# Performance work log

Hardware: AMD Instinct MI355X
Metric: run time of the kernel (lower is better)

The kernel has to match this reference:

```python
import jax, jax.numpy as jnp
import numpy as np

B, C, H, W = 8, 256, 64, 64
D = C // 8  # query/key channels


def setup_inputs() -> dict:
    key = jax.random.key(0)
    ks = jax.random.split(key, 7)
    s = 0.05
    x = jax.random.normal(ks[0], (B, C, H, W), dtype=jnp.float32)
    Wq = jax.random.normal(ks[1], (D, C), dtype=jnp.float32) * s
    bq = jax.random.normal(ks[2], (D,), dtype=jnp.float32) * s
    Wk = jax.random.normal(ks[3], (D, C), dtype=jnp.float32) * s
    bk = jax.random.normal(ks[4], (D,), dtype=jnp.float32) * s
    Wv = jax.random.normal(ks[5], (C, C), dtype=jnp.float32) * s
    bv = jax.random.normal(ks[6], (C,), dtype=jnp.float32) * s
    return {"x": x, "Wq": Wq, "bq": bq, "Wk": Wk, "bk": bk, "Wv": Wv, "bv": bv}


def reference(x, Wq, bq, Wk, bk, Wv, bv):
    b, c, h, w = x.shape
    n = h * w
    xf = x.reshape(b, c, n)  # (B, C, HW)
    # 1x1 convs == per-pixel linear projections
    q = jnp.einsum('dc,bcn->bdn', Wq, xf) + bq[None, :, None]  # (B, D, HW)
    k = jnp.einsum('dc,bcn->bdn', Wk, xf) + bk[None, :, None]  # (B, D, HW)
    v = jnp.einsum('ec,bcn->ben', Wv, xf) + bv[None, :, None]  # (B, C, HW)
    # attention[b, n, m] = sum_d q[b,d,n] * k[b,d,m]  (no 1/sqrt(d) scaling)
    attn = jax.nn.softmax(jnp.einsum('bdn,bdm->bnm', q, k), axis=-1)
    # out[b,c,n] = sum_m v[b,c,m] * attn[b,n,m]  (v @ attn^T)
    out = jnp.einsum('bcm,bnm->bcn', v, attn)
    return out.reshape(b, c, h, w) + x
```

## Files before the change

### kernel.cpp

```cpp
#include <hip/hip_runtime.h>
#include <stdint.h>

#define BN 4096
#define NCH 256
#define DQ 32

typedef _Float16 half8  __attribute__((ext_vector_type(8)));
typedef _Float16 half4  __attribute__((ext_vector_type(4)));
typedef _Float16 half2  __attribute__((ext_vector_type(2)));
typedef float   floatx4  __attribute__((ext_vector_type(4)));
typedef float   floatx16 __attribute__((ext_vector_type(16)));

typedef __attribute__((address_space(1))) const void g1_void;
typedef __attribute__((address_space(3))) void l3_void;

#define LOG2E 1.44269504088896f
#define EXP2F(x) __builtin_amdgcn_exp2f(x)
#define LOG2F(x) __builtin_amdgcn_logf(x)

__global__ __launch_bounds__(256) void convert_w(
    const float* __restrict__ Wq, const float* __restrict__ Wk,
    const float* __restrict__ Wv, _Float16* __restrict__ W16)
{
    int e4 = (blockIdx.x * 256 + threadIdx.x) * 4;
    float4 v;
    if (e4 < 8192)        v = *(const float4*)&Wq[e4];
    else if (e4 < 16384) {
        v = *(const float4*)&Wk[e4 - 8192];
        v.x *= LOG2E; v.y *= LOG2E; v.z *= LOG2E; v.w *= LOG2E;
    }
    else                  v = *(const float4*)&Wv[e4 - 16384];
    half4 h = { (_Float16)v.x, (_Float16)v.y, (_Float16)v.z, (_Float16)v.w };
    *(half4*)&W16[e4] = h;
}

__global__ __launch_bounds__(512) void proj_kernel(
    const float* __restrict__ x, const _Float16* __restrict__ W16,
    const float* __restrict__ bq, const float* __restrict__ bk,
    const float* __restrict__ bv,
    _Float16* __restrict__ qT, _Float16* __restrict__ kT,
    _Float16* __restrict__ vb)
{
    const int t  = threadIdx.x;
    const int n0 = blockIdx.x * 128;
    const int b  = blockIdx.y;

    __shared__ __align__(16) _Float16 xTl[128 * 256];

#pragma unroll
    for (int p = 0; p < 2; ++p) {
        const int kb = p * 128 + (t >> 5) * 8;
        const int n4 = (t & 31) * 4;
        float4 xr[8];
#pragma unroll
        for (int i = 0; i < 8; ++i)
            xr[i] = *(const float4*)&x[((size_t)b * NCH + kb + i) * BN + n0 + n4];
        const float* xf = (const float*)xr;
#pragma unroll
        for (int j = 0; j < 4; ++j) {
            const int n = n4 + j;
            half8 hv;
#pragma unroll
            for (int i = 0; i < 8; ++i) hv[i] = (_Float16)xf[i * 4 + j];
            const int phys = (kb >> 3) ^ ((n >> 2) & 31);
            *(half8*)&xTl[n * 256 + phys * 8] = hv;
        }
    }
    __syncthreads();

    const int lane  = t & 63;
    const int w     = t >> 6;
    const int col32 = lane & 31;
    const int h     = lane >> 5;
    const int nc    = w & 3;
    const int job   = w >> 2;

    const _Float16* Wq16 = W16;
    const _Float16* Wk16 = W16 + 8192;
    const _Float16* Wv16 = W16 + 16384;

#define XFRAG(ks) (*(const half8*)&xTl[(nc * 32 + col32) * 256 + \
        (((ks) * 2 + h) ^ (((nc * 32 + col32) >> 2) & 31)) * 8])

    if (job == 0) {
        const float bqv = bq[col32];
        const float bkv = bk[col32] * LOG2E;
        floatx16 aq, ak2;
#pragma unroll
        for (int r = 0; r < 16; ++r) { aq[r] = 0.0f; ak2[r] = 0.0f; }
#pragma unroll
        for (int ks = 0; ks < 16; ++ks) {
            half8 xa = XFRAG(ks);
            half8 wqf = *(const half8*)&Wq16[col32 * 256 + ks * 16 + h * 8];
            half8 wkf = *(const half8*)&Wk16[col32 * 256 + ks * 16 + h * 8];
            aq  = __builtin_amdgcn_mfma_f32_32x32x16_f16(xa, wqf, aq, 0, 0, 0);
            ak2 = __builtin_amdgcn_mfma_f32_32x32x16_f16(xa, wkf, ak2, 0, 0, 0);
        }
#pragma unroll
        for (int r = 0; r < 16; ++r) {
            const int n = n0 + nc * 32 + (r & 3) + 8 * (r >> 2) + 4 * h;
            qT[((size_t)b * BN + n) * DQ + col32] = (_Float16)(aq[r] + bqv);
            kT[((size_t)b * BN + n) * DQ + col32] = (_Float16)(ak2[r] + bkv);
        }
    }

    const int rg_lo = (job == 0) ? 0 : 3;
    const int rg_hi = (job == 0) ? 3 : 8;
    for (int rg = rg_lo; rg < rg_hi; ++rg) {
        floatx16 av;
#pragma unroll
        for (int r = 0; r < 16; ++r) av[r] = 0.0f;
#pragma unroll
        for (int ks = 0; ks < 16; ++ks) {
            half8 xb  = XFRAG(ks);
            half8 wvf = *(const half8*)&Wv16[(rg * 32 + col32) * 256 + ks * 16 + h * 8];
            av = __builtin_amdgcn_mfma_f32_32x32x16_f16(wvf, xb, av, 0, 0, 0);
        }
#pragma unroll
        for (int r = 0; r < 16; ++r) {
            const int c = rg * 32 + (r & 3) + 8 * (r >> 2) + 4 * h;
            vb[((size_t)b * NCH + c) * BN + n0 + nc * 32 + col32] =
                (_Float16)(av[r] + bv[c]);
        }
    }
#undef XFRAG
}

__global__ __launch_bounds__(256, 3) void flash_kernel(
    const _Float16* __restrict__ qT, const _Float16* __restrict__ kT,
    const _Float16* __restrict__ vb,
    _Float16* __restrict__ Op, float* __restrict__ Ml, int KPS)
{
    const int t    = threadIdx.x;
    const int lane = t & 63;
    const int w    = t >> 6;
    const int n0   = blockIdx.x * 64;
    const int kh   = blockIdx.y;
    const int b    = blockIdx.z;
    const int kbase = kh * KPS;
    const int iters = (min(KPS, BN - kbase)) >> 6;

    __shared__ __align__(16) _Float16 vs[NCH * 64];
    __shared__ __align__(16) _Float16 Ps[2][64 * 64];
    __shared__ float alph_s[2][64];
    __shared__ float l_s[64];

    const int col   = lane & 15;
    const int q4    = lane >> 4;
    const int col32 = lane & 31;
    const int h     = lane >> 5;

    const _Float16* kp = kT + (size_t)b * BN * DQ;
    const _Float16* vp = vb + (size_t)b * NCH * BN;

    half8 bqf = *(const half8*)&qT[((size_t)b * BN + n0 + w * 16 + col) * DQ + q4 * 8];

    floatx16 acc[2][2];
#pragma unroll
    for (int ct = 0; ct < 2; ++ct)
#pragma unroll
        for (int nt = 0; nt < 2; ++nt)
#pragma unroll
            for (int r = 0; r < 16; ++r) acc[ct][nt][r] = 0.0f;

    float m_i = -1e30f, l_i = 0.0f;

    const int sc_loc = lane >> 3;
    const int s_log  = (lane & 7) ^ (sc_loc & 7);
    half8 ak[4];
#pragma unroll
    for (int mt = 0; mt < 4; ++mt)
        ak[mt] = *(const half8*)&kp[(size_t)(kbase + mt * 16 + col) * DQ + q4 * 8];
#pragma unroll
    for (int j = 0; j < 8; ++j) {
        const int c = w * 64 + j * 8 + sc_loc;
        __builtin_amdgcn_global_load_lds(
            (g1_void*)&vp[(size_t)c * BN + kbase + s_log * 8],
            (l3_void*)&vs[(w * 64 + j * 8) * 64], 16, 0, 0);
    }

    for (int it = 0; it < iters; ++it) {
        const int mc  = kbase + it * 64;
        const int cur = it & 1;

        floatx4 sf[4];
        __builtin_amdgcn_s_setprio(1);
#pragma unroll
        for (int mt = 0; mt < 4; ++mt) {
            floatx4 z = { 0.0f, 0.0f, 0.0f, 0.0f };
            sf[mt] = __builtin_amdgcn_mfma_f32_16x16x32_f16(ak[mt], bqf, z, 0, 0, 0);
        }
        __builtin_amdgcn_s_setprio(0);

        {
            const int mcn = (it + 1 < iters) ? mc + 64 : mc;
#pragma unroll
            for (int mt = 0; mt < 4; ++mt)
                ak[mt] = *(const half8*)&kp[(size_t)(mcn + mt * 16 + col) * DQ + q4 * 8];
        }

        float cmax = -1e30f;
#pragma unroll
        for (int mt = 0; mt < 4; ++mt)
#pragma unroll
            for (int r = 0; r < 4; ++r) cmax = fmaxf(cmax, sf[mt][r]);
        cmax = fmaxf(cmax, __shfl_xor(cmax, 16));
        cmax = fmaxf(cmax, __shfl_xor(cmax, 32));
        const float mn = (cmax > m_i + 8.0f) ? cmax : m_i;
        float al = EXP2F(m_i - mn);
        float csum = 0.0f;
        half4 pk[4];
#pragma unroll
        for (int mt = 0; mt < 4; ++mt) {
            float p0 = EXP2F(sf[mt][0] - mn);
            float p1 = EXP2F(sf[mt][1] - mn);
            float p2 = EXP2F(sf[mt][2] - mn);
            float p3 = EXP2F(sf[mt][3] - mn);
            csum += p0 + p1 + p2 + p3;
            half2 q01 = __builtin_bit_cast(half2, __builtin_amdgcn_cvt_pkrtz(p0, p1));
            half2 q23 = __builtin_bit_cast(half2, __builtin_amdgcn_cvt_pkrtz(p2, p3));
            half4 pkv;
            pkv[0] = q01[0]; pkv[1] = q01[1];
            pkv[2] = q23[0]; pkv[3] = q23[1];
            pk[mt] = pkv;
        }
        csum += __shfl_xor(csum, 16);
        csum += __shfl_xor(csum, 32);
        l_i = l_i * al + csum;
        m_i = mn;

        {
            const int n = w * 16 + col;
#pragma unroll
            for (int mt = 0; mt < 4; ++mt) {
                const int p_log = 2 * mt + (q4 >> 1);
                const int p_phys = p_log ^ (n & 7);
                *(half4*)((char*)&Ps[cur][n * 64] + p_phys * 16 + (q4 & 1) * 8) = pk[mt];
            }
            if (q4 == 0) alph_s[cur][n] = al;
        }

        asm volatile("s_waitcnt lgkmcnt(0)" ::: "memory");
        __builtin_amdgcn_s_barrier();

        float a0 = alph_s[cur][col32];
        float a1 = alph_s[cur][32 + col32];
        if (!__all((a0 == 1.0f) && (a1 == 1.0f))) {
#pragma unroll
            for (int ct = 0; ct < 2; ++ct)
#pragma unroll
                for (int r = 0; r < 16; ++r) {
                    acc[ct][0][r] *= a0;
                    acc[ct][1][r] *= a1;
                }
        }

        asm volatile("s_waitcnt vmcnt(4)" ::: "memory");

        __builtin_amdgcn_s_setprio(1);
#pragma unroll
        for (int ks = 0; ks < 4; ++ks) {
            const int p_log = 2 * ks + h;
            half8 bp0 = *(const half8*)((char*)&Ps[cur][col32 * 64] + (p_log ^ (col32 & 7)) * 16);
            half8 bp1 = *(const half8*)((char*)&Ps[cur][(32 + col32) * 64] + (p_log ^ (col32 & 7)) * 16);
#pragma unroll
            for (int ct = 0; ct < 2; ++ct) {
                const int c = w * 64 + ct * 32 + col32;
                half8 av = *(const half8*)((char*)&vs[c * 64] + ((p_log ^ (c & 7)) * 16));
                acc[ct][0] = __builtin_amdgcn_mfma_f32_32x32x16_f16(av, bp0, acc[ct][0], 0, 0, 0);
                acc[ct][1] = __builtin_amdgcn_mfma_f32_32x32x16_f16(av, bp1, acc[ct][1], 0, 0, 0);
            }
        }
        __builtin_amdgcn_s_setprio(0);

        if (it + 1 < iters) {
            asm volatile("s_waitcnt lgkmcnt(0)" ::: "memory");
            const int mcn = mc + 64;
#pragma unroll
            for (int j = 0; j < 8; ++j) {
                const int c = w * 64 + j * 8 + sc_loc;
                __builtin_amdgcn_global_load_lds(
                    (g1_void*)&vp[(size_t)c * BN + mcn + s_log * 8],
                    (l3_void*)&vs[(w * 64 + j * 8) * 64], 16, 0, 0);
            }
        }
    }

    if (q4 == 0) {
        const int n = w * 16 + col;
        l_s[n] = l_i;
        Ml[(size_t)(kh * 8 + b) * BN + n0 + n] = m_i + LOG2F(l_i);
    }
    __syncthreads();
    const float li0 = 1.0f / l_s[col32];
    const float li1 = 1.0f / l_s[32 + col32];

    _Float16* Opp = Op + (size_t)(kh * 8 + b) * NCH * BN;
#pragma unroll
    for (int ct = 0; ct < 2; ++ct)
#pragma unroll
        for (int nt = 0; nt < 2; ++nt) {
            const float li = nt ? li1 : li0;
#pragma unroll
            for (int r = 0; r < 16; ++r) {
                int row = (r & 3) + 8 * (r >> 2) + 4 * h;
                int c = w * 64 + ct * 32 + row;
                Opp[(size_t)c * BN + n0 + nt * 32 + col32] = (_Float16)(acc[ct][nt][r] * li);
            }
        }
}

__global__ __launch_bounds__(256) void combine_kernel(
    const _Float16* __restrict__ Op, const float* __restrict__ Ml,
    const float* __restrict__ x, float* __restrict__ out, int nsplit)
{
    const int n  = (blockIdx.x * 256 + threadIdx.x) * 8;
    const int c0 = blockIdx.y * 16;
    const int b  = blockIdx.z;

    float f[3][8];
    float Z[8];
#pragma unroll
    for (int j = 0; j < 8; ++j) Z[j] = -1e30f;
    for (int s = 0; s < nsplit; ++s) {
        const float* mlp = &Ml[(size_t)(s * 8 + b) * BN + n];
        floatx4 z0 = *(const floatx4*)mlp;
        floatx4 z1 = *(const floatx4*)(mlp + 4);
#pragma unroll
        for (int j = 0; j < 4; ++j) { f[s][j] = z0[j]; f[s][4 + j] = z1[j]; }
#pragma unroll
        for (int j = 0; j < 8; ++j) Z[j] = fmaxf(Z[j], f[s][j]);
    }
    float lsum[8];
#pragma unroll
    for (int j = 0; j < 8; ++j) lsum[j] = 0.0f;
    for (int s = 0; s < nsplit; ++s)
#pragma unroll
        for (int j = 0; j < 8; ++j) { f[s][j] = EXP2F(f[s][j] - Z[j]); lsum[j] += f[s][j]; }
#pragma unroll
    for (int j = 0; j < 8; ++j) lsum[j] = 1.0f / lsum[j];
    for (int s = 0; s < nsplit; ++s)
#pragma unroll
        for (int j = 0; j < 8; ++j) f[s][j] *= lsum[j];

#pragma unroll 2
    for (int ci = 0; ci < 16; ++ci) {
        const int c = c0 + ci;
        const size_t off = ((size_t)b * NCH + c) * BN + n;
        const size_t po = (size_t)c * BN + n;
        float ov[8];
#pragma unroll
        for (int j = 0; j < 8; ++j) ov[j] = 0.0f;
        for (int s = 0; s < nsplit; ++s) {
            half8 hv = *(const half8*)&Op[(size_t)(s * 8 + b) * NCH * BN + po];
#pragma unroll
            for (int j = 0; j < 8; ++j) ov[j] += (float)hv[j] * f[s][j];
        }
        floatx4 x0 = *(const floatx4*)&x[off];
        floatx4 x1 = *(const floatx4*)&x[off + 4];
        floatx4 o0, o1;
#pragma unroll
        for (int j = 0; j < 4; ++j) { o0[j] = ov[j] + x0[j]; o1[j] = ov[4 + j] + x1[j]; }
        *(floatx4*)&out[off] = o0;
        *(floatx4*)&out[off + 4] = o1;
    }
}

extern "C" void kernel_launch(void* const* d_in, const int* in_sizes, int n_in,
                              void* d_out, int out_size, void* d_ws, size_t ws_size,
                              hipStream_t stream)
{
    const float* x  = (const float*)d_in[0];
    const float* Wq = (const float*)d_in[1];
    const float* bq = (const float*)d_in[2];
    const float* Wk = (const float*)d_in[3];
    const float* bk = (const float*)d_in[4];
    const float* Wv = (const float*)d_in[5];
    const float* bv = (const float*)d_in[6];
    float* out = (float*)d_out;

    _Float16* ws = (_Float16*)d_ws;
    _Float16* W16 = ws;
    _Float16* qT  = W16 + 81920;
    _Float16* kT  = qT + (size_t)8 * BN * DQ;
    _Float16* vb  = kT + (size_t)8 * BN * DQ;
    _Float16* Op  = vb + (size_t)8 * NCH * BN;

    const size_t baseElems = 81920 + (size_t)2 * 8 * BN * DQ + (size_t)8 * NCH * BN;
    const size_t opElems3  = (size_t)3 * 8 * NCH * BN;
    const size_t mlBytes   = (size_t)24 * BN * sizeof(float);
    const size_t need3     = (baseElems + opElems3) * 2 + mlBytes + 256;
    const int nsplit = (ws_size >= need3) ? 3 : 2;
    const int KPS    = (nsplit == 3) ? 1408 : 2048;

    float* Ml = (float*)(Op + (size_t)nsplit * 8 * NCH * BN);

    convert_w<<<dim3(80), 256, 0, stream>>>(Wq, Wk, Wv, W16);
    proj_kernel<<<dim3(32, 8), 512, 0, stream>>>(x, W16, bq, bk, bv, qT, kT, vb);
    flash_kernel<<<dim3(64, nsplit, 8), 256, 0, stream>>>(qT, kT, vb, Op, Ml, KPS);
    combine_kernel<<<dim3(2, 16, 8), 256, 0, stream>>>(Op, Ml, x, out, nsplit);
}
```

Before: 245.3 us.

## Software-pipeline flash loop so QK/softmax overlaps PV, widen combine grid

Restructures the flash attention inner loop into a prologue, steady state and epilogue. The QK MFMA and softmax for tile it+1 now run alongside the PV MFMAs for tile it, using the double-buffered P in LDS, which lets matrix work overlap with exp/reduction work within a wave. Separately, the combine kernel now handles 2 channels per block instead of 16, giving eight times more blocks for better occupancy but recomputing the split-normalisation weights more often. The pipelining adds register pressure from keeping sf/pk live across PV.

```diff
diff --git a/kernel.cpp b/kernel.cpp
--- a/kernel.cpp
+++ b/kernel.cpp
@@ -167,123 +167,148 @@
 
     const int sc_loc = lane >> 3;
     const int s_log  = (lane & 7) ^ (sc_loc & 7);
+
     half8 ak[4];
-#pragma unroll
-    for (int mt = 0; mt < 4; ++mt)
-        ak[mt] = *(const half8*)&kp[(size_t)(kbase + mt * 16 + col) * DQ + q4 * 8];
-#pragma unroll
-    for (int j = 0; j < 8; ++j) {
-        const int c = w * 64 + j * 8 + sc_loc;
-        __builtin_amdgcn_global_load_lds(
-            (g1_void*)&vp[(size_t)c * BN + kbase + s_log * 8],
-            (l3_void*)&vs[(w * 64 + j * 8) * 64], 16, 0, 0);
-    }
-
-    for (int it = 0; it < iters; ++it) {
-        const int mc  = kbase + it * 64;
-        const int cur = it & 1;
-
-        floatx4 sf[4];
-        __builtin_amdgcn_s_setprio(1);
-#pragma unroll
-        for (int mt = 0; mt < 4; ++mt) {
-            floatx4 z = { 0.0f, 0.0f, 0.0f, 0.0f };
-            sf[mt] = __builtin_amdgcn_mfma_f32_16x16x32_f16(ak[mt], bqf, z, 0, 0, 0);
-        }
-        __builtin_amdgcn_s_setprio(0);
-
-        {
-            const int mcn = (it + 1 < iters) ? mc + 64 : mc;
-#pragma unroll
-            for (int mt = 0; mt < 4; ++mt)
-                ak[mt] = *(const half8*)&kp[(size_t)(mcn + mt * 16 + col) * DQ + q4 * 8];
-        }
-
-        float cmax = -1e30f;
-#pragma unroll
-        for (int mt = 0; mt < 4; ++mt)
-#pragma unroll
-            for (int r = 0; r < 4; ++r) cmax = fmaxf(cmax, sf[mt][r]);
-        cmax = fmaxf(cmax, __shfl_xor(cmax, 16));
-        cmax = fmaxf(cmax, __shfl_xor(cmax, 32));
-        const float mn = (cmax > m_i + 8.0f) ? cmax : m_i;
-        float al = EXP2F(m_i - mn);
-        float csum = 0.0f;
-        half4 pk[4];
-#pragma unroll
-        for (int mt = 0; mt < 4; ++mt) {
-            float p0 = EXP2F(sf[mt][0] - mn);
-            float p1 = EXP2F(sf[mt][1] - mn);
-            float p2 = EXP2F(sf[mt][2] - mn);
-            float p3 = EXP2F(sf[mt][3] - mn);
-            csum += p0 + p1 + p2 + p3;
-            half2 q01 = __builtin_bit_cast(half2, __builtin_amdgcn_cvt_pkrtz(p0, p1));
-            half2 q23 = __builtin_bit_cast(half2, __builtin_amdgcn_cvt_pkrtz(p2, p3));
-            half4 pkv;
-            pkv[0] = q01[0]; pkv[1] = q01[1];
-            pkv[2] = q23[0]; pkv[3] = q23[1];
-            pk[mt] = pkv;
-        }
-        csum += __shfl_xor(csum, 16);
-        csum += __shfl_xor(csum, 32);
-        l_i = l_i * al + csum;
-        m_i = mn;
-
-        {
-            const int n = w * 16 + col;
-#pragma unroll
-            for (int mt = 0; mt < 4; ++mt) {
-                const int p_log = 2 * mt + (q4 >> 1);
-                const int p_phys = p_log ^ (n & 7);
-                *(half4*)((char*)&Ps[cur][n * 64] + p_phys * 16 + (q4 & 1) * 8) = pk[mt];
-            }
-            if (q4 == 0) alph_s[cur][n] = al;
-        }
-
+    floatx4 sf[4];
+    half4 pk[4];
+    float al;
+
+#define K_LOAD(MC)                                                          \
+    do {                                                                    \
+        _Pragma("unroll")                                                   \
+        for (int mt = 0; mt < 4; ++mt)                                      \
+            ak[mt] = *(const half8*)&kp[(size_t)((MC) + mt * 16 + col) * DQ + q4 * 8]; \
+    } while (0)
+
+#define V_DMA(MC)                                                           \
+    do {                                                                    \
+        _Pragma("unroll")                                                   \
+        for (int j = 0; j < 8; ++j) {                                       \
+            const int c = w * 64 + j * 8 + sc_loc;                          \
+            __builtin_amdgcn_global_load_lds(                               \
+                (g1_void*)&vp[(size_t)c * BN + (MC) + s_log * 8],           \
+                (l3_void*)&vs[(w * 64 + j * 8) * 64], 16, 0, 0);            \
+        }                                                                   \
+    } while (0)
+
+#define QK_STEP()                                                           \
+    do {                                                                    \
+        __builtin_amdgcn_s_setprio(1);                                      \
+        _Pragma("unroll")                                                   \
+        for (int mt = 0; mt < 4; ++mt) {                                    \
+            floatx4 z = { 0.0f, 0.0f, 0.0f, 0.0f };                         \
+            sf[mt] = __builtin_amdgcn_mfma_f32_16x16x32_f16(ak[mt], bqf, z, 0, 0, 0); \
+        }                                                                   \
+        __builtin_amdgcn_s_setprio(0);                                      \
+    } while (0)
+
+#define SM_STEP()                                                           \
+    do {                                                                    \
+        float cmax = -1e30f;                                                \
+        _Pragma("unroll")                                                   \
+        for (int mt = 0; mt < 4; ++mt)                                      \
+            _Pragma("unroll")                                               \
+            for (int r = 0; r < 4; ++r) cmax = fmaxf(cmax, sf[mt][r]);      \
+        cmax = fmaxf(cmax, __shfl_xor(cmax, 16));                           \
+        cmax = fmaxf(cmax, __shfl_xor(cmax, 32));                           \
+        const float mn = (cmax > m_i + 8.0f) ? cmax : m_i;                  \
+        al = EXP2F(m_i - mn);                                               \
+        float csum = 0.0f;                                                  \
+        _Pragma("unroll")                                                   \
+        for (int mt = 0; mt < 4; ++mt) {                                    \
+            float p0 = EXP2F(sf[mt][0] - mn);                               \
+            float p1 = EXP2F(sf[mt][1] - mn);                               \
+            float p2 = EXP2F(sf[mt][2] - mn);                               \
+            float p3 = EXP2F(sf[mt][3] - mn);                               \
+            csum += p0 + p1 + p2 + p3;                                      \
+            half2 q01 = __builtin_bit_cast(half2, __builtin_amdgcn_cvt_pkrtz(p0, p1)); \
+            half2 q23 = __builtin_bit_cast(half2, __builtin_amdgcn_cvt_pkrtz(p2, p3)); \
+            pk[mt][0] = q01[0]; pk[mt][1] = q01[1];                         \
+            pk[mt][2] = q23[0]; pk[mt][3] = q23[1];                         \
+        }                                                                   \
+        csum += __shfl_xor(csum, 16);                                       \
+        csum += __shfl_xor(csum, 32);                                       \
+        l_i = l_i * al + csum;                                              \
+        m_i = mn;                                                           \
+    } while (0)
+
+#define PS_WRITE(BUF)                                                       \
+    do {                                                                    \
+        const int n = w * 16 + col;                                         \
+        _Pragma("unroll")                                                   \
+        for (int mt = 0; mt < 4; ++mt) {                                    \
+            const int p_log = 2 * mt + (q4 >> 1);                           \
+            const int p_phys = p_log ^ (n & 7);                             \
+            *(half4*)((char*)&Ps[BUF][n * 64] + p_phys * 16 + (q4 & 1) * 8) = pk[mt]; \
+        }                                                                   \
+        if (q4 == 0) alph_s[BUF][n] = al;                                   \
+    } while (0)
+
+#define RESCALE(BUF)                                                        \
+    do {                                                                    \
+        float a0 = alph_s[BUF][col32];                                      \
+        float a1 = alph_s[BUF][32 + col32];                                 \
+        if (!__all((a0 == 1.0f) && (a1 == 1.0f))) {                         \
+            _Pragma("unroll")                                               \
+            for (int ct = 0; ct < 2; ++ct)                                  \
+                _Pragma("unroll")                                           \
+                for (int r = 0; r < 16; ++r) {                              \
+                    acc[ct][0][r] *= a0;                                    \
+                    acc[ct][1][r] *= a1;                                    \
+                }                                                           \
+        }                                                                   \
+    } while (0)
+
+#define PV_STEP(BUF)                                                        \
+    do {                                                                    \
+        __builtin_amdgcn_s_setprio(1);                                      \
+        _Pragma("unroll")                                                   \
+        for (int ks = 0; ks < 4; ++ks) {                                    \
+            const int p_log = 2 * ks + h;                                   \
+            half8 bp0 = *(const half8*)((char*)&Ps[BUF][col32 * 64] + (p_log ^ (col32 & 7)) * 16); \
+            half8 bp1 = *(const half8*)((char*)&Ps[BUF][(32 + col32) * 64] + (p_log ^ (col32 & 7)) * 16); \
+            _Pragma("unroll")                                               \
+            for (int ct = 0; ct < 2; ++ct) {                                \
+                const int c = w * 64 + ct * 32 + col32;                     \
+                half8 av = *(const half8*)((char*)&vs[c * 64] + ((p_log ^ (c & 7)) * 16)); \
+                acc[ct][0] = __builtin_amdgcn_mfma_f32_32x32x16_f16(av, bp0, acc[ct][0], 0, 0, 0); \
+                acc[ct][1] = __builtin_amdgcn_mfma_f32_32x32x16_f16(av, bp1, acc[ct][1], 0, 0, 0); \
+            }                                                               \
+        }                                                                   \
+        __builtin_amdgcn_s_setprio(0);                                      \
+    } while (0)
+
+    K_LOAD(kbase);
+    V_DMA(kbase);
+    QK_STEP();
+    { const int m1 = (1 < iters) ? kbase + 64 : kbase; K_LOAD(m1); }
+    SM_STEP();
+    PS_WRITE(0);
+
+    for (int it = 0; it < iters - 1; ++it) {
+        const int cur = it & 1, nxt = cur ^ 1;
         asm volatile("s_waitcnt lgkmcnt(0)" ::: "memory");
         __builtin_amdgcn_s_barrier();
-
-        float a0 = alph_s[cur][col32];
-        float a1 = alph_s[cur][32 + col32];
-        if (!__all((a0 == 1.0f) && (a1 == 1.0f))) {
-#pragma unroll
-            for (int ct = 0; ct < 2; ++ct)
-#pragma unroll
-                for (int r = 0; r < 16; ++r) {
-                    acc[ct][0][r] *= a0;
-                    acc[ct][1][r] *= a1;
-                }
-        }
-
+        QK_STEP();
+        { const int m2 = (it + 2 < iters) ? kbase + (it + 2) * 64
+                                          : kbase + (iters - 1) * 64;
+          K_LOAD(m2); }
+        RESCALE(cur);
         asm volatile("s_waitcnt vmcnt(4)" ::: "memory");
-
-        __builtin_amdgcn_s_setprio(1);
-#pragma unroll
-        for (int ks = 0; ks < 4; ++ks) {
-            const int p_log = 2 * ks + h;
-            half8 bp0 = *(const half8*)((char*)&Ps[cur][col32 * 64] + (p_log ^ (col32 & 7)) * 16);
-            half8 bp1 = *(const half8*)((char*)&Ps[cur][(32 + col32) * 64] + (p_log ^ (col32 & 7)) * 16);
-#pragma unroll
-            for (int ct = 0; ct < 2; ++ct) {
-                const int c = w * 64 + ct * 32 + col32;
-                half8 av = *(const half8*)((char*)&vs[c * 64] + ((p_log ^ (c & 7)) * 16));
-                acc[ct][0] = __builtin_amdgcn_mfma_f32_32x32x16_f16(av, bp0, acc[ct][0], 0, 0, 0);
-                acc[ct][1] = __builtin_amdgcn_mfma_f32_32x32x16_f16(av, bp1, acc[ct][1], 0, 0, 0);
-            }
-        }
-        __builtin_amdgcn_s_setprio(0);
-
-        if (it + 1 < iters) {
-            asm volatile("s_waitcnt lgkmcnt(0)" ::: "memory");
-            const int mcn = mc + 64;
-#pragma unroll
-            for (int j = 0; j < 8; ++j) {
-                const int c = w * 64 + j * 8 + sc_loc;
-                __builtin_amdgcn_global_load_lds(
-                    (g1_void*)&vp[(size_t)c * BN + mcn + s_log * 8],
-                    (l3_void*)&vs[(w * 64 + j * 8) * 64], 16, 0, 0);
-            }
-        }
+        PV_STEP(cur);
+        SM_STEP();
+        PS_WRITE(nxt);
+        asm volatile("s_waitcnt lgkmcnt(0)" ::: "memory");
+        V_DMA(kbase + (it + 1) * 64);
+    }
+
+    {
+        const int cur = (iters - 1) & 1;
+        asm volatile("s_waitcnt lgkmcnt(0)" ::: "memory");
+        __builtin_amdgcn_s_barrier();
+        RESCALE(cur);
+        asm volatile("s_waitcnt vmcnt(0)" ::: "memory");
+        PV_STEP(cur);
     }
 
     if (q4 == 0) {
@@ -308,6 +333,13 @@
                 Opp[(size_t)c * BN + n0 + nt * 32 + col32] = (_Float16)(acc[ct][nt][r] * li);
             }
         }
+#undef K_LOAD
+#undef V_DMA
+#undef QK_STEP
+#undef SM_STEP
+#undef PS_WRITE
+#undef RESCALE
+#undef PV_STEP
 }
 
 __global__ __launch_bounds__(256) void combine_kernel(
@@ -315,7 +347,7 @@
     const float* __restrict__ x, float* __restrict__ out, int nsplit)
 {
     const int n  = (blockIdx.x * 256 + threadIdx.x) * 8;
-    const int c0 = blockIdx.y * 16;
+    const int c0 = blockIdx.y * 2;
     const int b  = blockIdx.z;
 
     float f[3][8];
@@ -344,7 +376,7 @@
         for (int j = 0; j < 8; ++j) f[s][j] *= lsum[j];
 
 #pragma unroll 2
-    for (int ci = 0; ci < 16; ++ci) {
+    for (int ci = 0; ci < 2; ++ci) {
         const int c = c0 + ci;
         const size_t off = ((size_t)b * NCH + c) * BN + n;
         const size_t po = (size_t)c * BN + n;
@@ -398,5 +430,5 @@
     convert_w<<<dim3(80), 256, 0, stream>>>(Wq, Wk, Wv, W16);
     proj_kernel<<<dim3(32, 8), 512, 0, stream>>>(x, W16, bq, bk, bv, qT, kT, vb);
     flash_kernel<<<dim3(64, nsplit, 8), 256, 0, stream>>>(qT, kT, vb, Op, Ml, KPS);
-    combine_kernel<<<dim3(2, 16, 8), 256, 0, stream>>>(Op, Ml, x, out, nsplit);
+    combine_kernel<<<dim3(2, 128, 8), 256, 0, stream>>>(Op, Ml, x, out, nsplit);
 }
```

New measurement: 237.5 us (median of 2 runs). -3.2%, faster.
